# Performance work log

Measured on AMD Instinct MI355X. Metric: run time of the kernel, lower is better.

Reference implementation:

```python
import jax, jax.numpy as jnp
import numpy as np

GRID = 64
N = GRID * GRID            # N_NODES = 4096
B = 8
IN_DIM = 12
HID = 64
HEADS = 4
HD = HID                    # per-head channels (GATConv(hidden, hidden, concat=False))
EDGE_DIM = 3
N_ODE_STEPS = 4             # fixed-step RK4 over t in [0, 1] (stands in for dopri5; 16 f-evals)


def _grid_edges():
    """8-neighborhood edges on the 64x64 grid + unit direction vectors."""
    idx = np.arange(N).reshape(GRID, GRID)
    srcs, dsts, dirs = [], [], []
    for dy in (-1, 0, 1):
        for dx in (-1, 0, 1):
            if dy == 0 and dx == 0:
                continue
            r0, r1 = max(0, -dy), GRID - max(0, dy)
            c0, c1 = max(0, -dx), GRID - max(0, dx)
            s = idx[r0:r1, c0:c1].ravel()
            d = idx[r0 + dy:r1 + dy, c0 + dx:c1 + dx].ravel()
            srcs.append(s)
            dsts.append(d)
            v = np.array([dx, dy], dtype=np.float32)
            v /= np.linalg.norm(v)
            dirs.append(np.tile(v, (s.size, 1)))
    edge_index = np.stack([np.concatenate(srcs), np.concatenate(dsts)], 0).astype(np.int32)
    edge_dirs = np.concatenate(dirs, 0).astype(np.float32)
    return jnp.asarray(edge_index), jnp.asarray(edge_dirs)


def _ln(x, g, b):
    m = x.mean(-1, keepdims=True)
    v = x.var(-1, keepdims=True)
    return (x - m) / jnp.sqrt(v + 1e-5) * g + b


def setup_inputs() -> dict:
    key = jax.random.key(0)
    ks = jax.random.split(key, 12)
    edge_index, edge_dirs = _grid_edges()
    x = jax.random.uniform(ks[0], (B, IN_DIM, GRID, GRID), jnp.float32)

    def lin(k, i, o):
        return jax.random.normal(k, (i, o), jnp.float32) / np.sqrt(i)

    return {
        "x": x,
        "edge_index": edge_index,
        "edge_dirs": edge_dirs,
        "W_enc1": lin(ks[1], IN_DIM, HID), "b_enc1": jnp.zeros((HID,), jnp.float32),
        "W_enc2": lin(ks[2], HID, HID), "b_enc2": jnp.zeros((HID,), jnp.float32),
        "W_gat": lin(ks[3], HID, HEADS * HD),
        "att_src": jax.random.normal(ks[4], (HEADS, HD), jnp.float32) / np.sqrt(HD),
        "att_dst": jax.random.normal(ks[5], (HEADS, HD), jnp.float32) / np.sqrt(HD),
        "W_edge": lin(ks[6], EDGE_DIM, HEADS * HD),
        "att_edge": jax.random.normal(ks[7], (HEADS, HD), jnp.float32) / np.sqrt(HD),
        "b_gat": jnp.zeros((HID,), jnp.float32),
        "g_f": jnp.ones((HID,), jnp.float32), "bt_f": jnp.zeros((HID,), jnp.float32),
        "g_h": jnp.ones((HID,), jnp.float32), "bt_h": jnp.zeros((HID,), jnp.float32),
        "W_h1": lin(ks[8], HID, HID), "b_h1": jnp.zeros((HID,), jnp.float32),
        "W_h2": lin(ks[9], HID, 1), "b_h2": jnp.zeros((1,), jnp.float32),
    }


def reference(x, edge_index, edge_dirs, W_enc1, b_enc1, W_enc2, b_enc2, W_gat,
              att_src, att_dst, W_edge, att_edge, b_gat, g_f, bt_f, g_h, bt_h,
              W_h1, b_h1, W_h2, b_h2):
    Bs = x.shape[0]
    E = edge_index.shape[1]
    BN = Bs * N
    nodes = x.reshape(Bs, IN_DIM, N).transpose(0, 2, 1)          # [B, N, 12]
    h = (jax.nn.silu(nodes @ W_enc1 + b_enc1) @ W_enc2 + b_enc2).reshape(BN, HID)

    src, dst = edge_index[0], edge_index[1]
    # edge features: unit direction (2) + fire-channel (ch 0) difference (1)
    diff = nodes[:, dst, 0] - nodes[:, src, 0]                    # [B, E]
    ea = jnp.concatenate(
        [jnp.broadcast_to(edge_dirs[None], (Bs, E, 2)), diff[..., None]], -1
    ).reshape(Bs * E, EDGE_DIM)
    off = (jnp.arange(Bs, dtype=src.dtype) * N)[:, None]
    bsrc = (src[None] + off).reshape(-1)                          # [B*E]
    bdst = (dst[None] + off).reshape(-1)

    # edge-conditioned attention term is constant over ODE time
    e_lin = (ea @ W_edge).reshape(-1, HEADS, HD)                  # [BE, H, C]
    a_edge = (e_lin * att_edge).sum(-1)                           # [BE, H]

    def f(hh):
        xl = (hh @ W_gat).reshape(BN, HEADS, HD)                  # [BN, H, C]
        a_s = (xl * att_src).sum(-1)                              # [BN, H]
        a_d = (xl * att_dst).sum(-1)
        a = jax.nn.leaky_relu(a_s[bsrc] + a_d[bdst] + a_edge, 0.2)
        amax = jax.ops.segment_max(a, bdst, num_segments=BN)      # per-destination softmax
        p = jnp.exp(a - amax[bdst])
        z = jax.ops.segment_sum(p, bdst, num_segments=BN)
        alpha = p / (z[bdst] + 1e-16)                             # [BE, H]
        msg = jax.ops.segment_sum(alpha[:, :, None] * xl[bsrc], bdst, num_segments=BN)
        out = msg.mean(1) + b_gat                                 # heads averaged (concat=False)
        return jax.nn.silu(_ln(out, g_f, bt_f))

    dt = 1.0 / N_ODE_STEPS
    for _ in range(N_ODE_STEPS):                                  # fixed small count: ok
        k1 = f(h)
        k2 = f(h + 0.5 * dt * k1)
        k3 = f(h + 0.5 * dt * k2)
        k4 = f(h + dt * k3)
        h = h + (dt / 6.0) * (k1 + 2.0 * k2 + 2.0 * k3 + k4)

    z = jax.nn.silu(_ln(h, g_h, bt_h) @ W_h1 + b_h1)
    logits = (z @ W_h2 + b_h2).reshape(Bs, GRID, GRID)
    init_fire = x[:, 0]
    logits = jnp.where(init_fire > 0.5, jnp.maximum(logits, 6.0), logits)
    return logits
```

## Files before the change

kernel.cpp:

```cpp
#include <hip/hip_runtime.h>

#define NN 4096
#define BN 32768

typedef __attribute__((ext_vector_type(8))) short short8;
typedef __attribute__((ext_vector_type(4))) float f32x4;

__device__ __forceinline__ float sigmoidf_(float x){ return 1.f/(1.f+__expf(-x)); }
__device__ __forceinline__ unsigned short bfr(float f){
    unsigned int u = __float_as_uint(f);
    u += 0x7FFFu + ((u>>16)&1u);
    return (unsigned short)(u>>16);
}
__device__ __forceinline__ float b2f(unsigned short h){
    return __uint_as_float(((unsigned int)h)<<16);
}

__global__ void prep_kernel(const float* __restrict__ W_gat,
                            const float* __restrict__ att_src,
                            const float* __restrict__ att_dst,
                            const float* __restrict__ W_edge,
                            const float* __restrict__ att_edge,
                            float* __restrict__ As, float* __restrict__ Ad,
                            float* __restrict__ cE,
                            unsigned short* __restrict__ AsAdT,
                            unsigned short* __restrict__ WT2h,
                            unsigned short* __restrict__ WT2l)
{
    int t = threadIdx.x;
    int i = t >> 2, hh = t & 3;
    float s = 0.f, d = 0.f;
    for (int j = 0; j < 64; j++){
        float w = W_gat[i*256 + hh*64 + j];
        s += w * att_src[hh*64 + j];
        d += w * att_dst[hh*64 + j];
    }
    As[t] = s;
    Ad[t] = d;
    if (t < 12){
        int e = t >> 2, h2 = t & 3;
        float cc = 0.f;
        for (int k = 0; k < 64; k++)
            cc += W_edge[e*256 + h2*64 + k] * att_edge[h2*64 + k];
        cE[h2*3 + e] = cc;
    }
    __syncthreads();
    if (t < 16){
        for (int k = 0; k < 64; k++){
            float v = (t < 4) ? As[k*4 + t] : (t < 8 ? Ad[k*4 + (t-4)] : 0.f);
            AsAdT[t*64 + k] = bfr(v);
        }
    }
    {
        int j = t >> 2, q = t & 3;
        for (int k = 0; k < 64; k++){
            float wv = W_gat[k*256 + q*64 + j];
            unsigned short hi = bfr(wv);
            WT2h[j*256 + q*64 + k] = hi;
            WT2l[j*256 + q*64 + k] = bfr(wv - b2f(hi));
        }
    }
}

__global__ __launch_bounds__(256) void enc_kernel(
    const float* __restrict__ x,
    const float* __restrict__ W1, const float* __restrict__ b1,
    const float* __restrict__ W2, const float* __restrict__ b2,
    float* __restrict__ H, float* __restrict__ HA)
{
    __shared__ __align__(16) float sm[5168];
    float* xT  = sm;
    float* t1  = sm + 816;

    int t = threadIdx.x;
    int w = __builtin_amdgcn_readfirstlane(t >> 6);
    int lane = t & 63;
    int n0 = blockIdx.x * 64;
    int b = n0 >> 12;
    int cell0 = n0 & 4095;

    for (int e = t; e < 12*64; e += 256){
        int c = e >> 6, u = e & 63;
        xT[c*68 + u] = x[b*(12*NN) + c*NN + cell0 + u];
    }
    __syncthreads();

    #pragma unroll
    for (int jj = 0; jj < 16; jj++){
        int j = w*16 + jj;
        float a = b1[j];
        #pragma unroll
        for (int c = 0; c < 12; c++)
            a += xT[c*68 + lane] * W1[c*64 + j];
        t1[j*68 + lane] = a * sigmoidf_(a);
    }
    __syncthreads();

    float hk[16];
    #pragma unroll
    for (int kk = 0; kk < 16; kk++) hk[kk] = b2[w*16 + kk];
    for (int j = 0; j < 64; j++){
        float v = t1[j*68 + lane];
        #pragma unroll
        for (int kk = 0; kk < 16; kk++)
            hk[kk] += v * W2[j*64 + w*16 + kk];
    }
    int hb = (n0 + lane)*64 + w*16;
    #pragma unroll
    for (int j4 = 0; j4 < 4; j4++){
        float4 v = make_float4(hk[4*j4+0], hk[4*j4+1], hk[4*j4+2], hk[4*j4+3]);
        *(float4*)&H[hb + 4*j4]  = v;
        *(float4*)&HA[hb + 4*j4] = v;
    }
}

__global__ __launch_bounds__(256,2) void f_kernel(
    const float* __restrict__ HINc,
    const float* __restrict__ x,
    const float* __restrict__ CCE,
    const unsigned short* __restrict__ AsAdT,
    const unsigned short* __restrict__ WT2h, const unsigned short* __restrict__ WT2l,
    const float* __restrict__ b_gat, const float* __restrict__ g_f, const float* __restrict__ bt_f,
    float* __restrict__ H, float* __restrict__ HOUT, float* __restrict__ ACC,
    int stage)
{
    __shared__ __align__(16) char smem[69632];
    float* as2 = (float*)(smem + 65536);
    float* ad2 = (float*)(smem + 67328);
    float* x0h = (float*)(smem + 69120);

    int t = threadIdx.x;
    int w = __builtin_amdgcn_readfirstlane(t >> 6);
    int lane = t & 63;
    int l15 = lane & 15, lg = lane >> 4;
    int blk = blockIdx.x;
    int b = blk & 7, tile = blk >> 3;
    int tr = tile >> 3, tc = tile & 7;
    int r0 = tr*8 - 1, c0 = tc*8 - 1;
    int nb = b*NN;
    int xb = b*(12*NN);

    const int DYI[8] = {-1,-1,-1,0,0,1,1,1};
    const int DXI[8] = {-1,0,1,-1,1,-1,0,1};
    const float s2c = 0.70710678f;
    const float DXN[8] = {-s2c,0.f,s2c,-1.f,1.f,-s2c,0.f,s2c};
    const float DYN[8] = {-s2c,-1.f,-s2c,0.f,0.f,s2c,1.f,s2c};

    for (int u = t; u < 1024; u += 256)
        *(float4*)(smem + 16384 + u*16) = make_float4(0.f,0.f,0.f,0.f);
    for (int u = t; u < 2048; u += 256){
        int m = u & 127, k4 = u >> 7;
        int k0 = k4*4;
        float4 v = make_float4(0.f,0.f,0.f,0.f);
        if (m < 100){
            int hr = m/10, hc = m - hr*10;
            int r = min(63,max(0,r0+hr)), c = min(63,max(0,c0+hc));
            v = *(const float4*)&HINc[(long)(nb + r*64 + c)*64 + k0];
            if (k4 == 0) x0h[m] = x[xb + r*64 + c];
        } else if (k4 == 0) x0h[m] = 0.f;
        *(unsigned short*)(smem + (((k0+0)*256 + m*2) ^ (((k0+0)&7)<<4))) = bfr(v.x);
        *(unsigned short*)(smem + (((k0+1)*256 + m*2) ^ (((k0+1)&7)<<4))) = bfr(v.y);
        *(unsigned short*)(smem + (((k0+2)*256 + m*2) ^ (((k0+2)&7)<<4))) = bfr(v.z);
        *(unsigned short*)(smem + (((k0+3)*256 + m*2) ^ (((k0+3)&7)<<4))) = bfr(v.w);
    }
    __syncthreads();

    for (int nt = w; nt < 7; nt += 4){
        int m = nt*16 + l15;
        int hr = m/10, hc = m - hr*10;
        int r = min(63,max(0,r0+hr)), c = min(63,max(0,c0+hc));
        const float* hp = &HINc[(long)(nb + r*64 + c)*64];
        f32x4 acc = {0.f,0.f,0.f,0.f};
        #pragma unroll
        for (int kt = 0; kt < 2; kt++){
            int k = kt*32 + lg*8;
            short8 afr = *(const short8*)&AsAdT[l15*64 + k];
            float4 f0 = *(const float4*)&hp[k];
            float4 f1 = *(const float4*)&hp[k+4];
            short8 bfrg;
            bfrg[0]=(short)bfr(f0.x); bfrg[1]=(short)bfr(f0.y);
            bfrg[2]=(short)bfr(f0.z); bfrg[3]=(short)bfr(f0.w);
            bfrg[4]=(short)bfr(f1.x); bfrg[5]=(short)bfr(f1.y);
            bfrg[6]=(short)bfr(f1.z); bfrg[7]=(short)bfr(f1.w);
            acc = __builtin_amdgcn_mfma_f32_16x16x32_bf16(afr, bfrg, acc, 0,0,0);
        }
        if (lg == 0)      *(float4*)&as2[m*4] = *(float4*)&acc;
        else if (lg == 1) *(float4*)&ad2[m*4] = *(float4*)&acc;
    }
    __syncthreads();

    int e = lane, hh = w;
    int er = e >> 3, ec = e & 7;
    int gr = tr*8 + er, gc = tc*8 + ec;
    int me = (er+1)*10 + (ec+1);
    float al[8]; int hmr[8];
    {
        float adv = ad2[me*4 + hh];
        float x0n = x0h[me];
        float ce0 = CCE[hh*3+0], ce1 = CCE[hh*3+1], ce2 = CCE[hh*3+2];
        float mx = -1e30f;
        #pragma unroll
        for (int o = 0; o < 8; o++){
            int mr = gr - DYI[o], mc = gc - DXI[o];
            bool vld = (mr>=0)&&(mr<64)&&(mc>=0)&&(mc<64);
            int hm = me - DYI[o]*10 - DXI[o];
            hmr[o] = hm;
            float a = as2[hm*4+hh] + adv + ce0*DXN[o] + ce1*DYN[o]
                    + ce2*(x0n - x0h[hm]);
            a = (a >= 0.f) ? a : 0.2f*a;
            al[o] = vld ? a : -1e30f;
            mx = fmaxf(mx, al[o]);
        }
        float z = 0.f;
        #pragma unroll
        for (int o = 0; o < 8; o++){
            float p = (al[o] > -1e29f) ? __expf(al[o]-mx) : 0.f;
            al[o] = p; z += p;
        }
        float zi = 1.f/(z + 1e-16f);
        #pragma unroll
        for (int o = 0; o < 8; o++) al[o] *= zi;
    }

    for (int h2 = 0; h2 < 4; ++h2){
        if (hh == h2){
            #pragma unroll
            for (int o = 0; o < 8; o++)
                *(unsigned short*)(smem + 16384 + ((e*256 + hmr[o]*2) ^ ((e&7)<<4)))
                    = bfr(al[o]);
        }
        __syncthreads();
        f32x4 sacc[4];
        #pragma unroll
        for (int nt = 0; nt < 4; nt++) sacc[nt] = (f32x4){0.f,0.f,0.f,0.f};
        #pragma unroll
        for (int kt = 0; kt < 4; kt++){
            int row = w*16 + l15;
            short8 afr = *(const short8*)(smem + 16384 +
                ((row*256 + (kt*32+lg*8)*2) ^ ((row&7)<<4)));
            #pragma unroll
            for (int nt = 0; nt < 4; nt++){
                int k2 = nt*16 + l15;
                short8 bfrg = *(const short8*)(smem +
                    ((k2*256 + (kt*32+lg*8)*2) ^ ((k2&7)<<4)));
                sacc[nt] = __builtin_amdgcn_mfma_f32_16x16x32_bf16(afr, bfrg, sacc[nt], 0,0,0);
            }
        }
        #pragma unroll
        for (int nt = 0; nt < 4; nt++){
            #pragma unroll
            for (int reg = 0; reg < 4; reg++){
                int e2 = w*16 + lg*4 + reg;
                int col = h2*64 + nt*16 + l15;
                *(unsigned short*)(smem + 32768 + ((e2*512 + col*2) ^ ((e2&7)<<4)))
                    = bfr(sacc[nt][reg]);
            }
        }
        __syncthreads();
    }

    f32x4 oacc[4];
    #pragma unroll
    for (int nt = 0; nt < 4; nt++) oacc[nt] = (f32x4){0.f,0.f,0.f,0.f};
    #pragma unroll
    for (int half = 0; half < 2; half++){
        const unsigned short* Wt = half ? WT2l : WT2h;
        #pragma unroll
        for (int kt = 0; kt < 8; kt++){
            int e2 = w*16 + l15;
            short8 afr = *(const short8*)(smem + 32768 +
                ((e2*512 + (kt*32+lg*8)*2) ^ ((e2&7)<<4)));
            #pragma unroll
            for (int nt = 0; nt < 4; nt++){
                short8 bfrg = *(const short8*)&Wt[(nt*16+l15)*256 + kt*32 + lg*8];
                oacc[nt] = __builtin_amdgcn_mfma_f32_16x16x32_bf16(afr, bfrg, oacc[nt], 0,0,0);
            }
        }
    }

    float bg[4], gf[4], bf[4];
    #pragma unroll
    for (int nt = 0; nt < 4; nt++){
        int j = nt*16 + l15;
        bg[nt] = b_gat[j]; gf[nt] = g_f[j]; bf[nt] = bt_f[j];
    }
    #pragma unroll
    for (int reg = 0; reg < 4; reg++){
        int e2 = w*16 + lg*4 + reg;
        float vv[4];
        float s1 = 0.f, s2 = 0.f;
        #pragma unroll
        for (int nt = 0; nt < 4; nt++){
            float v = oacc[nt][reg]*0.25f + bg[nt];
            vv[nt] = v; s1 += v; s2 += v*v;
        }
        s1 += __shfl_xor(s1,1); s2 += __shfl_xor(s2,1);
        s1 += __shfl_xor(s1,2); s2 += __shfl_xor(s2,2);
        s1 += __shfl_xor(s1,4); s2 += __shfl_xor(s2,4);
        s1 += __shfl_xor(s1,8); s2 += __shfl_xor(s2,8);
        float mean = s1*(1.f/64.f);
        float var  = s2*(1.f/64.f) - mean*mean;
        float rstd = rsqrtf(fmaxf(var,0.f) + 1e-5f);
        int r2 = e2 >> 3, c2 = e2 & 7;
        long gn = nb + (tr*8 + r2)*64 + (tc*8 + c2);
        #pragma unroll
        for (int nt = 0; nt < 4; nt++){
            int j = nt*16 + l15;
            float y = (vv[nt]-mean)*rstd*gf[nt] + bf[nt];
            float kv = y * sigmoidf_(y);
            long idx = gn*64 + j;
            float hold = H[idx];
            float hn;
            if (stage == 0){
                ACC[idx] = kv;                 hn = hold + 0.125f*kv;
            } else if (stage == 1){
                ACC[idx] += 2.f*kv;            hn = hold + 0.125f*kv;
            } else if (stage == 2){
                ACC[idx] += 2.f*kv;            hn = hold + 0.25f*kv;
            } else {
                hn = hold + (0.25f/6.f)*(ACC[idx] + kv);
                H[idx] = hn;
            }
            HOUT[idx] = hn;
        }
    }
}

__global__ __launch_bounds__(256) void head_kernel(
    const float* __restrict__ H, const float* __restrict__ x,
    const float* __restrict__ g_h, const float* __restrict__ bt_h,
    const float* __restrict__ Wh1, const float* __restrict__ bh1,
    const float* __restrict__ Wh2, const float* __restrict__ bh2,
    float* __restrict__ out)
{
    __shared__ __align__(16) float sm[4624];
    float* hT = sm;
    float* pl = sm + 4352;

    int t = threadIdx.x;
    int w = __builtin_amdgcn_readfirstlane(t >> 6);
    int lane = t & 63;
    int n0 = blockIdx.x * 64;
    int b = n0 >> 12;
    int cell0 = n0 & 4095;

    for (int e = t; e < 4096; e += 256){
        int n = e >> 6, j = e & 63;
        hT[j*68 + n] = H[(n0+n)*64 + j];
    }
    __syncthreads();

    float s1 = 0.f, s2 = 0.f;
    for (int j = 0; j < 64; j++){
        float v = hT[j*68 + lane];
        s1 += v; s2 += v*v;
    }
    float mean = s1*(1.f/64.f);
    float var  = s2*(1.f/64.f) - mean*mean;
    float rstd = rsqrtf(fmaxf(var, 0.f) + 1e-5f);

    float acc[16];
    #pragma unroll
    for (int kk = 0; kk < 16; kk++) acc[kk] = bh1[w*16 + kk];
    for (int j = 0; j < 64; j++){
        float v = (hT[j*68 + lane] - mean)*rstd*g_h[j] + bt_h[j];
        #pragma unroll
        for (int kk = 0; kk < 16; kk++)
            acc[kk] += v * Wh1[j*64 + w*16 + kk];
    }
    float plg = 0.f;
    #pragma unroll
    for (int kk = 0; kk < 16; kk++){
        float a = acc[kk];
        plg += (a * sigmoidf_(a)) * Wh2[w*16 + kk];
    }
    pl[w*68 + lane] = plg;
    __syncthreads();
    if (t < 64){
        float lgt = pl[0*68+t] + pl[1*68+t] + pl[2*68+t] + pl[3*68+t] + bh2[0];
        float fire = x[b*(12*NN) + cell0 + t];
        out[n0 + t] = (fire > 0.5f) ? fmaxf(lgt, 6.f) : lgt;
    }
}

extern "C" void kernel_launch(void* const* d_in, const int* in_sizes, int n_in,
                              void* d_out, int out_size, void* d_ws, size_t ws_size,
                              hipStream_t stream)
{
    const float* x       = (const float*)d_in[0];
    const float* W_enc1  = (const float*)d_in[3];
    const float* b_enc1  = (const float*)d_in[4];
    const float* W_enc2  = (const float*)d_in[5];
    const float* b_enc2  = (const float*)d_in[6];
    const float* W_gat   = (const float*)d_in[7];
    const float* att_src = (const float*)d_in[8];
    const float* att_dst = (const float*)d_in[9];
    const float* W_edge  = (const float*)d_in[10];
    const float* att_edge= (const float*)d_in[11];
    const float* b_gat   = (const float*)d_in[12];
    const float* g_f     = (const float*)d_in[13];
    const float* bt_f    = (const float*)d_in[14];
    const float* g_h     = (const float*)d_in[15];
    const float* bt_h    = (const float*)d_in[16];
    const float* W_h1    = (const float*)d_in[17];
    const float* b_h1    = (const float*)d_in[18];
    const float* W_h2    = (const float*)d_in[19];
    const float* b_h2    = (const float*)d_in[20];

    float* ws  = (float*)d_ws;
    float* H   = ws;
    float* HA  = ws + 2097152;
    float* HB  = ws + 4194304;
    float* ACC = ws + 6291456;
    float* CAS = ws + 8388608;
    float* CAD = ws + 8388864;
    float* CCE = ws + 8389120;
    unsigned short* AsAdT = (unsigned short*)(ws + 8389376);
    unsigned short* WT2h  = (unsigned short*)(ws + 8389888);
    unsigned short* WT2l  = (unsigned short*)(ws + 8398080);
    float* out = (float*)d_out;

    prep_kernel<<<1, 256, 0, stream>>>(W_gat, att_src, att_dst, W_edge, att_edge,
                                       CAS, CAD, CCE, AsAdT, WT2h, WT2l);
    enc_kernel<<<512, 256, 0, stream>>>(x, W_enc1, b_enc1, W_enc2, b_enc2, H, HA);

    float* hin = HA; float* hout = HB;
    for (int step = 0; step < 4; step++){
        for (int st = 0; st < 4; st++){
            f_kernel<<<512, 256, 0, stream>>>(hin, x, CCE, AsAdT, WT2h, WT2l,
                                              b_gat, g_f, bt_f,
                                              H, hout, ACC, st);
            float* tm = hin; hin = hout; hout = tm;
        }
    }

    head_kernel<<<512, 256, 0, stream>>>(H, x, g_h, bt_h, W_h1, b_h1, W_h2, b_h2, out);
}
```

Before: 554.0 us.

## Replace dense attention-matrix MFMA aggregation with sparse 8-neighbor FMA gather

Drops the dense 64x100 attention matrix and the per-head MFMA products with their head-serialised barriers. Each thread now gathers its 8 neighbours' bf16 halo features directly, weighted by all four heads' alphas, with plain FMAs into registers. The halo features are staged once in a padded row-major bf16 layout, which also feeds the attention-logit MFMA instead of re-reading global memory. Shared memory drops from about 68KB to about 29KB and the occupancy hint is removed, at the cost of a large register array (G[8][8]) that may limit occupancy or spill.

```diff
diff --git a/kernel.cpp b/kernel.cpp
--- a/kernel.cpp
+++ b/kernel.cpp
@@ -114,7 +114,7 @@
     }
 }
 
-__global__ __launch_bounds__(256,2) void f_kernel(
+__global__ __launch_bounds__(256) void f_kernel(
     const float* __restrict__ HINc,
     const float* __restrict__ x,
     const float* __restrict__ CCE,
@@ -124,10 +124,12 @@
     float* __restrict__ H, float* __restrict__ HOUT, float* __restrict__ ACC,
     int stage)
 {
-    __shared__ __align__(16) char smem[69632];
-    float* as2 = (float*)(smem + 65536);
-    float* ad2 = (float*)(smem + 67328);
-    float* x0h = (float*)(smem + 69120);
+    __shared__ __align__(16) char smem[29376];
+    unsigned short* hA = (unsigned short*)smem;
+    float* aL  = (float*)(smem + 16128);
+    float* as2 = (float*)(smem + 25344);
+    float* ad2 = (float*)(smem + 27136);
+    float* x0h = (float*)(smem + 28928);
 
     int t = threadIdx.x;
     int w = __builtin_amdgcn_readfirstlane(t >> 6);
@@ -146,66 +148,49 @@
     const float DXN[8] = {-s2c,0.f,s2c,-1.f,1.f,-s2c,0.f,s2c};
     const float DYN[8] = {-s2c,-1.f,-s2c,0.f,0.f,s2c,1.f,s2c};
 
-    for (int u = t; u < 1024; u += 256)
-        *(float4*)(smem + 16384 + u*16) = make_float4(0.f,0.f,0.f,0.f);
-    for (int u = t; u < 2048; u += 256){
-        int m = u & 127, k4 = u >> 7;
-        int k0 = k4*4;
-        float4 v = make_float4(0.f,0.f,0.f,0.f);
-        if (m < 100){
-            int hr = m/10, hc = m - hr*10;
-            int r = min(63,max(0,r0+hr)), c = min(63,max(0,c0+hc));
-            v = *(const float4*)&HINc[(long)(nb + r*64 + c)*64 + k0];
-            if (k4 == 0) x0h[m] = x[xb + r*64 + c];
-        } else if (k4 == 0) x0h[m] = 0.f;
-        *(unsigned short*)(smem + (((k0+0)*256 + m*2) ^ (((k0+0)&7)<<4))) = bfr(v.x);
-        *(unsigned short*)(smem + (((k0+1)*256 + m*2) ^ (((k0+1)&7)<<4))) = bfr(v.y);
-        *(unsigned short*)(smem + (((k0+2)*256 + m*2) ^ (((k0+2)&7)<<4))) = bfr(v.z);
-        *(unsigned short*)(smem + (((k0+3)*256 + m*2) ^ (((k0+3)&7)<<4))) = bfr(v.w);
-    }
-    __syncthreads();
-
-    for (int nt = w; nt < 7; nt += 4){
-        int m = nt*16 + l15;
+    for (int u = t; u < 432; u += 256)
+        ((unsigned int*)(smem + 14400))[u] = 0u;
+    for (int u = t; u < 1600; u += 256){
+        int m = u >> 4, k4 = u & 15;
         int hr = m/10, hc = m - hr*10;
         int r = min(63,max(0,r0+hr)), c = min(63,max(0,c0+hc));
-        const float* hp = &HINc[(long)(nb + r*64 + c)*64];
+        float4 v = *(const float4*)&HINc[(long)(nb + r*64 + c)*64 + k4*4];
+        unsigned int p0 = (unsigned int)bfr(v.x) | ((unsigned int)bfr(v.y)<<16);
+        unsigned int p1 = (unsigned int)bfr(v.z) | ((unsigned int)bfr(v.w)<<16);
+        *(uint2*)&hA[m*72 + k4*4] = make_uint2(p0,p1);
+        if (k4 == 0) x0h[m] = x[xb + r*64 + c];
+    }
+    __syncthreads();
+
+    for (int nt = w; nt < 7; nt += 4){
         f32x4 acc = {0.f,0.f,0.f,0.f};
         #pragma unroll
         for (int kt = 0; kt < 2; kt++){
-            int k = kt*32 + lg*8;
-            short8 afr = *(const short8*)&AsAdT[l15*64 + k];
-            float4 f0 = *(const float4*)&hp[k];
-            float4 f1 = *(const float4*)&hp[k+4];
-            short8 bfrg;
-            bfrg[0]=(short)bfr(f0.x); bfrg[1]=(short)bfr(f0.y);
-            bfrg[2]=(short)bfr(f0.z); bfrg[3]=(short)bfr(f0.w);
-            bfrg[4]=(short)bfr(f1.x); bfrg[5]=(short)bfr(f1.y);
-            bfrg[6]=(short)bfr(f1.z); bfrg[7]=(short)bfr(f1.w);
+            short8 afr  = *(const short8*)&AsAdT[l15*64 + kt*32 + lg*8];
+            short8 bfrg = *(const short8*)&hA[(nt*16+l15)*72 + kt*32 + lg*8];
             acc = __builtin_amdgcn_mfma_f32_16x16x32_bf16(afr, bfrg, acc, 0,0,0);
         }
-        if (lg == 0)      *(float4*)&as2[m*4] = *(float4*)&acc;
-        else if (lg == 1) *(float4*)&ad2[m*4] = *(float4*)&acc;
-    }
-    __syncthreads();
-
-    int e = lane, hh = w;
-    int er = e >> 3, ec = e & 7;
-    int gr = tr*8 + er, gc = tc*8 + ec;
-    int me = (er+1)*10 + (ec+1);
-    float al[8]; int hmr[8];
+        int m = nt*16 + l15;
+        if (lg == 0)      *(float4*)&as2[m*4] = make_float4(acc[0],acc[1],acc[2],acc[3]);
+        else if (lg == 1) *(float4*)&ad2[m*4] = make_float4(acc[0],acc[1],acc[2],acc[3]);
+    }
+    __syncthreads();
+
     {
-        float adv = ad2[me*4 + hh];
+        int e = lane;
+        int er = e >> 3, ec = e & 7;
+        int gr = tr*8 + er, gc = tc*8 + ec;
+        int me = (er+1)*10 + (ec+1);
+        float adv = ad2[me*4 + w];
         float x0n = x0h[me];
-        float ce0 = CCE[hh*3+0], ce1 = CCE[hh*3+1], ce2 = CCE[hh*3+2];
-        float mx = -1e30f;
+        float ce0 = CCE[w*3+0], ce1 = CCE[w*3+1], ce2 = CCE[w*3+2];
+        float al[8]; float mx = -1e30f;
         #pragma unroll
         for (int o = 0; o < 8; o++){
             int mr = gr - DYI[o], mc = gc - DXI[o];
             bool vld = (mr>=0)&&(mr<64)&&(mc>=0)&&(mc<64);
             int hm = me - DYI[o]*10 - DXI[o];
-            hmr[o] = hm;
-            float a = as2[hm*4+hh] + adv + ce0*DXN[o] + ce1*DYN[o]
+            float a = as2[hm*4+w] + adv + ce0*DXN[o] + ce1*DYN[o]
                     + ce2*(x0n - x0h[hm]);
             a = (a >= 0.f) ? a : 0.2f*a;
             al[o] = vld ? a : -1e30f;
@@ -219,74 +204,66 @@
         }
         float zi = 1.f/(z + 1e-16f);
         #pragma unroll
-        for (int o = 0; o < 8; o++) al[o] *= zi;
-    }
-
-    for (int h2 = 0; h2 < 4; ++h2){
-        if (hh == h2){
-            #pragma unroll
-            for (int o = 0; o < 8; o++)
-                *(unsigned short*)(smem + 16384 + ((e*256 + hmr[o]*2) ^ ((e&7)<<4)))
-                    = bfr(al[o]);
-        }
-        __syncthreads();
-        f32x4 sacc[4];
-        #pragma unroll
-        for (int nt = 0; nt < 4; nt++) sacc[nt] = (f32x4){0.f,0.f,0.f,0.f};
-        #pragma unroll
-        for (int kt = 0; kt < 4; kt++){
-            int row = w*16 + l15;
-            short8 afr = *(const short8*)(smem + 16384 +
-                ((row*256 + (kt*32+lg*8)*2) ^ ((row&7)<<4)));
-            #pragma unroll
-            for (int nt = 0; nt < 4; nt++){
-                int k2 = nt*16 + l15;
-                short8 bfrg = *(const short8*)(smem +
-                    ((k2*256 + (kt*32+lg*8)*2) ^ ((k2&7)<<4)));
-                sacc[nt] = __builtin_amdgcn_mfma_f32_16x16x32_bf16(afr, bfrg, sacc[nt], 0,0,0);
-            }
-        }
+        for (int o = 0; o < 8; o++)
+            aL[e*36 + o*4 + w] = al[o]*zi;
+    }
+    __syncthreads();
+
+    int e2 = w*16 + l15;
+    int er2 = e2 >> 3, ec2 = e2 & 7;
+    int me2 = (er2+1)*10 + (ec2+1);
+    float G[8][8];
+    #pragma unroll
+    for (int kt = 0; kt < 8; kt++)
+        #pragma unroll
+        for (int i = 0; i < 8; i++) G[kt][i] = 0.f;
+    #pragma unroll
+    for (int o = 0; o < 8; o++){
+        int hm = me2 - DYI[o]*10 - DXI[o];
+        float4 ao = *(const float4*)&aL[e2*36 + o*4];
+        const unsigned short* hp = &hA[hm*72 + lg*8];
+        short8 v0 = *(const short8*)&hp[0];
+        short8 v1 = *(const short8*)&hp[32];
+        #pragma unroll
+        for (int i = 0; i < 8; i++){
+            float f0 = b2f((unsigned short)v0[i]);
+            float f1 = b2f((unsigned short)v1[i]);
+            G[0][i] += ao.x*f0;  G[1][i] += ao.x*f1;
+            G[2][i] += ao.y*f0;  G[3][i] += ao.y*f1;
+            G[4][i] += ao.z*f0;  G[5][i] += ao.z*f1;
+            G[6][i] += ao.w*f0;  G[7][i] += ao.w*f1;
+        }
+    }
+
+    f32x4 oacc[4];
+    #pragma unroll
+    for (int nt = 0; nt < 4; nt++) oacc[nt] = (f32x4){0.f,0.f,0.f,0.f};
+    #pragma unroll
+    for (int kt = 0; kt < 8; kt++){
+        short8 afr;
+        #pragma unroll
+        for (int i = 0; i < 8; i++) afr[i] = (short)bfr(G[kt][i]);
         #pragma unroll
         for (int nt = 0; nt < 4; nt++){
-            #pragma unroll
-            for (int reg = 0; reg < 4; reg++){
-                int e2 = w*16 + lg*4 + reg;
-                int col = h2*64 + nt*16 + l15;
-                *(unsigned short*)(smem + 32768 + ((e2*512 + col*2) ^ ((e2&7)<<4)))
-                    = bfr(sacc[nt][reg]);
-            }
-        }
-        __syncthreads();
-    }
-
-    f32x4 oacc[4];
-    #pragma unroll
-    for (int nt = 0; nt < 4; nt++) oacc[nt] = (f32x4){0.f,0.f,0.f,0.f};
-    #pragma unroll
-    for (int half = 0; half < 2; half++){
-        const unsigned short* Wt = half ? WT2l : WT2h;
-        #pragma unroll
-        for (int kt = 0; kt < 8; kt++){
-            int e2 = w*16 + l15;
-            short8 afr = *(const short8*)(smem + 32768 +
-                ((e2*512 + (kt*32+lg*8)*2) ^ ((e2&7)<<4)));
-            #pragma unroll
-            for (int nt = 0; nt < 4; nt++){
-                short8 bfrg = *(const short8*)&Wt[(nt*16+l15)*256 + kt*32 + lg*8];
-                oacc[nt] = __builtin_amdgcn_mfma_f32_16x16x32_bf16(afr, bfrg, oacc[nt], 0,0,0);
-            }
-        }
-    }
-
-    float bg[4], gf[4], bf[4];
+            short8 bh = *(const short8*)&WT2h[(nt*16+l15)*256 + kt*32 + lg*8];
+            oacc[nt] = __builtin_amdgcn_mfma_f32_16x16x32_bf16(afr, bh, oacc[nt], 0,0,0);
+        }
+        #pragma unroll
+        for (int nt = 0; nt < 4; nt++){
+            short8 bl = *(const short8*)&WT2l[(nt*16+l15)*256 + kt*32 + lg*8];
+            oacc[nt] = __builtin_amdgcn_mfma_f32_16x16x32_bf16(afr, bl, oacc[nt], 0,0,0);
+        }
+    }
+
+    float bg[4], gf[4], bf_[4];
     #pragma unroll
     for (int nt = 0; nt < 4; nt++){
         int j = nt*16 + l15;
-        bg[nt] = b_gat[j]; gf[nt] = g_f[j]; bf[nt] = bt_f[j];
+        bg[nt] = b_gat[j]; gf[nt] = g_f[j]; bf_[nt] = bt_f[j];
     }
     #pragma unroll
     for (int reg = 0; reg < 4; reg++){
-        int e2 = w*16 + lg*4 + reg;
+        int e3 = w*16 + lg*4 + reg;
         float vv[4];
         float s1 = 0.f, s2 = 0.f;
         #pragma unroll
@@ -301,12 +278,12 @@
         float mean = s1*(1.f/64.f);
         float var  = s2*(1.f/64.f) - mean*mean;
         float rstd = rsqrtf(fmaxf(var,0.f) + 1e-5f);
-        int r2 = e2 >> 3, c2 = e2 & 7;
+        int r2 = e3 >> 3, c2 = e3 & 7;
         long gn = nb + (tr*8 + r2)*64 + (tc*8 + c2);
         #pragma unroll
         for (int nt = 0; nt < 4; nt++){
             int j = nt*16 + l15;
-            float y = (vv[nt]-mean)*rstd*gf[nt] + bf[nt];
+            float y = (vv[nt]-mean)*rstd*gf[nt] + bf_[nt];
             float kv = y * sigmoidf_(y);
             long idx = gn*64 + j;
             float hold = H[idx];
```

New measurement: 512.6 us. -7.5%, faster.
